# Kernel tuning notes

Hardware: AMD Instinct MI355X
Metric: run time of the kernel (lower is better)

## Reference

```python
import jax, jax.numpy as jnp
import numpy as np

B, S, D, H, L = 2, 2048, 512, 8, 4
DK = D // H
FFN = 2048
CHUNK, LEFT, RIGHT = 64, 128, 32
EPS = 1e-3  # keras LayerNormalization default epsilon
NEG_INF = -1.0e9


def _banded_mask():
    # chunk-local emformer mask: row i in chunk c attends to [c*CHUNK-LEFT, (c+1)*CHUNK+RIGHT)
    m = np.zeros((S, S), np.int32)
    for c in range(S // CHUNK):
        r0, r1 = c * CHUNK, (c + 1) * CHUNK
        c0, c1 = max(0, r0 - LEFT), min(S, r1 + RIGHT)
        m[r0:r1, c0:c1] = 1
    return jnp.asarray(np.broadcast_to(m[None, None], (B, 1, S, S)))


def setup_inputs() -> dict:
    key = jax.random.key(0)
    ks = jax.random.split(key, 8)
    sd = 1.0 / np.sqrt(D)
    inp = {
        "x": jax.random.normal(ks[0], (B, S, D), jnp.float32),
        "mask": _banded_mask(),
        "Wq": jax.random.normal(ks[1], (L, D, D), jnp.float32) * sd,
        "bq": jnp.zeros((L, D), jnp.float32),
        "Wk": jax.random.normal(ks[2], (L, D, D), jnp.float32) * sd,
        "bk": jnp.zeros((L, D), jnp.float32),
        "Wv": jax.random.normal(ks[3], (L, D, D), jnp.float32) * sd,
        "bv": jnp.zeros((L, D), jnp.float32),
        "W1": jax.random.normal(ks[4], (L, D, FFN), jnp.float32) * sd,
        "b1": jnp.zeros((L, FFN), jnp.float32),
        "W2": jax.random.normal(ks[5], (L, FFN, D), jnp.float32) / np.sqrt(FFN),
        "b2": jnp.zeros((L, D), jnp.float32),
        "ln_in_g": jnp.ones((L, D), jnp.float32),
        "ln_in_b": jnp.zeros((L, D), jnp.float32),
        "ln1_g": jnp.ones((L, D), jnp.float32),
        "ln1_b": jnp.zeros((L, D), jnp.float32),
        "ln2_g": jnp.ones((L, D), jnp.float32),
        "ln2_b": jnp.zeros((L, D), jnp.float32),
    }
    return inp


def _ln(x, g, b):
    mu = jnp.mean(x, axis=-1, keepdims=True)
    var = jnp.mean(jnp.square(x - mu), axis=-1, keepdims=True)
    return (x - mu) * jax.lax.rsqrt(var + EPS) * g + b


def _block(x, maskf, Wq, bq, Wk, bk, Wv, bv, W1, b1, W2, b2, g_in, b_in, g1, bb1, g2, bb2):
    bs = x.shape[0]
    xl = _ln(x, g_in, b_in)
    q = (xl @ Wq + bq).reshape(bs, -1, H, DK).transpose(0, 2, 1, 3)  # [B,H,S,dk]
    k = (xl @ Wk + bk).reshape(bs, -1, H, DK).transpose(0, 2, 1, 3)
    v = (xl @ Wv + bv).reshape(bs, -1, H, DK).transpose(0, 2, 1, 3)
    scores = jnp.einsum("bhsd,bhtd->bhst", q, k) / np.sqrt(DK)
    scores = scores + NEG_INF * (1.0 - maskf)
    probs = jax.nn.softmax(scores, axis=-1)
    out = jnp.einsum("bhst,bhtd->bhsd", probs, v)
    out = out.transpose(0, 2, 1, 3).reshape(bs, -1, H * DK)
    out = out + x  # residual to block input (pre-LN)
    attn_out = _ln(out, g1, bb1)
    ffn = jax.nn.relu(attn_out @ W1 + b1) @ W2 + b2
    return _ln(ffn + attn_out, g2, bb2)


def reference(x, mask, Wq, bq, Wk, bk, Wv, bv, W1, b1, W2, b2,
              ln_in_g, ln_in_b, ln1_g, ln1_b, ln2_g, ln2_b):
    maskf = mask.astype(x.dtype)
    for i in range(L):
        x = _block(x, maskf, Wq[i], bq[i], Wk[i], bk[i], Wv[i], bv[i],
                   W1[i], b1[i], W2[i], b2[i],
                   ln_in_g[i], ln_in_b[i], ln1_g[i], ln1_b[i], ln2_g[i], ln2_b[i])
    return x
```

## Files before the change

### kernel.cpp

```cpp
#include <hip/hip_runtime.h>
#include <stdint.h>

#define DEVI __device__ __forceinline__

typedef __attribute__((ext_vector_type(8))) short bf16x8;
typedef __attribute__((ext_vector_type(4))) float f32x4;

DEVI short tobf(float v){
  uint32_t u = __builtin_bit_cast(uint32_t, v);
  uint32_t r = (u + 0x7fffu + ((u >> 16) & 1u)) >> 16;
  return (short)(uint16_t)r;
}

DEVI float frombf(short s){
  uint32_t u = ((uint32_t)(uint16_t)s) << 16;
  return __builtin_bit_cast(float, u);
}

DEVI f32x4 mfma16(bf16x8 a, bf16x8 b, f32x4 c){
  return __builtin_amdgcn_mfma_f32_16x16x32_bf16(a, b, c, 0, 0, 0);
}

DEVI void async16(const void* g, void* lds_uniform){
  __builtin_amdgcn_global_load_lds(
      (const __attribute__((address_space(1))) unsigned int*)g,
      (__attribute__((address_space(3))) unsigned int*)lds_uniform,
      16, 0, 0);
}

DEVI void ln_row_compute(const float* __restrict__ in, const short* __restrict__ inb,
                         const float* __restrict__ resf, const short* __restrict__ resb,
                         const float* __restrict__ g, const float* __restrict__ be,
                         const float* __restrict__ gn, const float* __restrict__ bn,
                         float* __restrict__ outf, short* __restrict__ outb, int row)
{
  const int lane = threadIdx.x & 63;
  const size_t base = (size_t)row * 512 + lane * 8;
  const int col = lane * 8;
  f32x4 x0, x1;
  if (in){
    x0 = *(const f32x4*)(in + base);
    x1 = *(const f32x4*)(in + base + 4);
  } else {
    bf16x8 ib = *(const bf16x8*)(inb + base);
    #pragma unroll
    for (int i = 0; i < 4; i++){ x0[i] = frombf(ib[i]); x1[i] = frombf(ib[i+4]); }
  }
  if (resf){
    f32x4 r0v = *(const f32x4*)(resf + base), r1v = *(const f32x4*)(resf + base + 4);
    x0 += r0v; x1 += r1v;
  }
  if (resb){
    bf16x8 rb = *(const bf16x8*)(resb + base);
    #pragma unroll
    for (int i = 0; i < 4; i++){ x0[i] += frombf(rb[i]); x1[i] += frombf(rb[i+4]); }
  }
  float s = x0[0]+x0[1]+x0[2]+x0[3]+x1[0]+x1[1]+x1[2]+x1[3];
  #pragma unroll
  for (int m = 1; m < 64; m <<= 1) s += __shfl_xor(s, m, 64);
  const float mu = s * (1.f/512.f);
  float vs = 0.f;
  #pragma unroll
  for (int i = 0; i < 4; i++){
    float d0 = x0[i]-mu; vs += d0*d0;
    float d1 = x1[i]-mu; vs += d1*d1;
  }
  #pragma unroll
  for (int m = 1; m < 64; m <<= 1) vs += __shfl_xor(vs, m, 64);
  const float rs = rsqrtf(vs * (1.f/512.f) + 1e-3f);
  f32x4 gv0 = *(const f32x4*)(g+col),  gv1 = *(const f32x4*)(g+col+4);
  f32x4 bv0 = *(const f32x4*)(be+col), bv1 = *(const f32x4*)(be+col+4);
  f32x4 y0, y1;
  #pragma unroll
  for (int i = 0; i < 4; i++){
    y0[i] = (x0[i]-mu)*rs*gv0[i] + bv0[i];
    y1[i] = (x1[i]-mu)*rs*gv1[i] + bv1[i];
  }
  if (outf){ *(f32x4*)(outf+base) = y0; *(f32x4*)(outf+base+4) = y1; }
  if (outb){
    f32x4 z0 = y0, z1 = y1;
    if (gn){
      float s2 = z0[0]+z0[1]+z0[2]+z0[3]+z1[0]+z1[1]+z1[2]+z1[3];
      #pragma unroll
      for (int m = 1; m < 64; m <<= 1) s2 += __shfl_xor(s2, m, 64);
      const float mu2 = s2 * (1.f/512.f);
      float v2 = 0.f;
      #pragma unroll
      for (int i = 0; i < 4; i++){
        float d0 = z0[i]-mu2; v2 += d0*d0;
        float d1 = z1[i]-mu2; v2 += d1*d1;
      }
      #pragma unroll
      for (int m = 1; m < 64; m <<= 1) v2 += __shfl_xor(v2, m, 64);
      const float rs2 = rsqrtf(v2 * (1.f/512.f) + 1e-3f);
      f32x4 gn0 = *(const f32x4*)(gn+col), gn1 = *(const f32x4*)(gn+col+4);
      f32x4 bn0 = *(const f32x4*)(bn+col), bn1 = *(const f32x4*)(bn+col+4);
      #pragma unroll
      for (int i = 0; i < 4; i++){
        z0[i] = (z0[i]-mu2)*rs2*gn0[i] + bn0[i];
        z1[i] = (z1[i]-mu2)*rs2*gn1[i] + bn1[i];
      }
    }
    bf16x8 ob;
    #pragma unroll
    for (int i = 0; i < 4; i++){ ob[i] = tobf(z0[i]); ob[i+4] = tobf(z1[i]); }
    *(bf16x8*)(outb + base) = ob;
  }
}

__global__ __launch_bounds__(256)
void transpose_all(const float* __restrict__ Wq, const float* __restrict__ Wk,
                   const float* __restrict__ Wv, const float* __restrict__ W1,
                   const float* __restrict__ W2,
                   short* __restrict__ WqkvT, short* __restrict__ W1T,
                   short* __restrict__ W2T,
                   const float* __restrict__ x_in, const float* __restrict__ gin,
                   const float* __restrict__ bin, short* __restrict__ xl)
{
  if (blockIdx.x >= 11264){
    const int row = ((blockIdx.x - 11264) << 2) + (threadIdx.x >> 6);
    ln_row_compute(x_in, nullptr, nullptr, nullptr, gin, bin,
                   nullptr, nullptr, nullptr, xl, row);
    return;
  }
  __shared__ float tsh[32][33];
  const int l = blockIdx.x / 2816;
  const int t = blockIdx.x % 2816;
  const float* src; short* dst; int K, N, local;
  if (t < 768){
    const int m = t >> 8;
    src = (m==0 ? Wq : (m==1 ? Wk : Wv)) + (size_t)l*262144;
    dst = WqkvT + (size_t)l*786432 + m*262144; K = 512; N = 512; local = t & 255;
  } else if (t < 1792){
    src = W1 + (size_t)l*1048576; dst = W1T + (size_t)l*1048576;
    K = 512; N = 2048; local = t - 768;
  } else {
    src = W2 + (size_t)l*1048576; dst = W2T + (size_t)l*1048576;
    K = 2048; N = 512; local = t - 1792;
  }
  const int tnx = N >> 5;
  const int tc = (local % tnx) << 5, tr = (local / tnx) << 5;
  const int lr = threadIdx.x >> 5, lc = threadIdx.x & 31;
  #pragma unroll
  for (int i = 0; i < 32; i += 8)
    tsh[lr + i][lc] = src[(size_t)(tr + lr + i) * N + tc + lc];
  __syncthreads();
  #pragma unroll
  for (int i = 0; i < 32; i += 8)
    dst[(size_t)(tc + lr + i) * K + tr + lc] = tobf(tsh[lc][lr + i]);
}

__global__ __launch_bounds__(256)
void ln_kernel(const float* __restrict__ in, const short* __restrict__ inb,
               const float* __restrict__ resf, const short* __restrict__ resb,
               const float* __restrict__ g, const float* __restrict__ be,
               const float* __restrict__ gn, const float* __restrict__ bn,
               float* __restrict__ outf, short* __restrict__ outb)
{
  const int row = (blockIdx.x << 2) + (threadIdx.x >> 6);
  ln_row_compute(in, inb, resf, resb, g, be, gn, bn, outf, outb, row);
}

template<int MODE, int BJ, int BK>
__global__ __launch_bounds__(256)
void gemm_bt(const short* __restrict__ A, const short* __restrict__ BT,
             int N, int K,
             const float* __restrict__ b0, const float* __restrict__ b1p,
             const float* __restrict__ b2p, void* __restrict__ out0)
{
  constexpr int NTILE = 32*BJ;
  constexpr int UPR = BK/8;
  constexpr int AU = 64*UPR/256;
  constexpr int BU = NTILE*UPR/256;
  __shared__ __align__(16) short Ash[64*BK];
  __shared__ __align__(16) short Bsh[NTILE*BK];
  const int tid = threadIdx.x;
  const int wid = tid >> 6, lane = tid & 63;
  const int l15 = lane & 15, g4 = lane >> 4;
  const int nbn = N / NTILE;
  const int cpx = gridDim.x >> 3;
  int bid = blockIdx.x;
  bid = (bid & 7) * cpx + (bid >> 3);
  const int bm = bid / nbn, bn = bid % nbn;
  const int m0 = bm << 6, n0 = bn * NTILE;

  const short* aP[AU]; const short* bP[BU];
  #pragma unroll
  for (int p = 0; p < AU; p++){
    int u = p*256 + tid, row = u / UPR, sl = (u % UPR) ^ (row & (UPR-1));
    aP[p] = A + (size_t)(m0 + row) * K + sl * 8;
  }
  #pragma unroll
  for (int p = 0; p < BU; p++){
    int u = p*256 + tid, row = u / UPR, sl = (u % UPR) ^ (row & (UPR-1));
    bP[p] = BT + (size_t)(n0 + row) * K + sl * 8;
  }
  char* ldsA = (char*)Ash;
  char* ldsB = (char*)Bsh;

  f32x4 acc[2][BJ] = {};
  const int wr = wid & 1, wc = wid >> 1;
  const int nkt = K / BK;

  for (int kt = 0; kt < nkt; ++kt){
    const int k0 = kt * BK;
    #pragma unroll
    for (int p = 0; p < AU; p++)
      async16(aP[p] + k0, ldsA + (p*256 + wid*64) * 16);
    #pragma unroll
    for (int p = 0; p < BU; p++)
      async16(bP[p] + k0, ldsB + (p*256 + wid*64) * 16);
    __syncthreads();
    #pragma unroll
    for (int ks = 0; ks < BK/32; ++ks){
      bf16x8 af[2], bfm[BJ];
      #pragma unroll
      for (int i = 0; i < 2; i++){
        const int ar = wr*32 + i*16 + l15;
        af[i] = *(const bf16x8*)&ldsA[ar*(2*BK) + (((ks<<2)+g4) ^ (ar&(UPR-1)))*16];
      }
      #pragma unroll
      for (int j = 0; j < BJ; j++){
        const int br = wc*(16*BJ) + j*16 + l15;
        bfm[j] = *(const bf16x8*)&ldsB[br*(2*BK) + (((ks<<2)+g4) ^ (br&(UPR-1)))*16];
      }
      #pragma unroll
      for (int i = 0; i < 2; i++)
        #pragma unroll
        for (int j = 0; j < BJ; j++)
          acc[i][j] = mfma16(af[i], bfm[j], acc[i][j]);
    }
    __syncthreads();
  }

  const int r0 = m0 + wr*32 + g4*4;
  const int cc0 = n0 + wc*16*BJ + l15;
  #pragma unroll
  for (int j = 0; j < BJ; j++){
    const int gc = cc0 + j*16;
    if (MODE == 0){
      const float bi = gc < 512 ? b0[gc] : (gc < 1024 ? b1p[gc-512] : b2p[gc-1024]);
      short* ob = (short*)out0;
      #pragma unroll
      for (int i = 0; i < 2; i++)
        #pragma unroll
        for (int r = 0; r < 4; r++){
          const int grow = r0 + i*16 + r;
          ob[(size_t)grow * N + gc] = tobf(acc[i][j][r] + bi);
        }
    } else {
      const float bi = b0[gc];
      short* ob = (short*)out0;
      #pragma unroll
      for (int i = 0; i < 2; i++)
        #pragma unroll
        for (int r = 0; r < 4; r++){
          const int grow = r0 + i*16 + r;
          float v = acc[i][j][r] + bi;
          v = fmaxf(v, 0.f);
          ob[(size_t)grow * N + gc] = tobf(v);
        }
    }
  }
}

__global__ __launch_bounds__(256)
void attn_kernel(const short* __restrict__ qkv, short* __restrict__ attnO,
                 const float* __restrict__ resid)
{
  constexpr int NT = 14, NK2 = 7, VS = 232, LDQ = 1536;
  __shared__ __align__(16) short Vt[64*VS];
  __shared__ __align__(16) short Pl[4][16*VS];
  const int c = blockIdx.x, h = blockIdx.y, b = blockIdx.z;
  const int kb0 = 64*c - 128;
  const size_t rowbase = (size_t)b*2048;
  const short* Q     = qkv + (rowbase + 64*c)*LDQ + h*64;
  const short* Kbase = qkv + rowbase*LDQ + 512  + h*64;
  const short* Vbase = qkv + rowbase*LDQ + 1024 + h*64;
  const int tid = threadIdx.x, wid = tid >> 6, lane = tid & 63;
  const int l15 = lane & 15, g4 = lane >> 4;

  for (int idx = tid; idx < NT*16*8; idx += 256){
    const int t = idx >> 7, rem = idx & 127;
    const int r = rem >> 3, d8 = (rem & 7) << 3;
    const int kb = kb0 + t*16;
    bf16x8 v = {0,0,0,0,0,0,0,0};
    if (kb >= 0 && kb + 16 <= 2048)
      v = *(const bf16x8*)(Vbase + (size_t)(kb + r)*LDQ + d8);
    short* dst = &Vt[d8*VS + t*16 + r];
    #pragma unroll
    for (int e = 0; e < 8; e++) dst[e*VS] = v[e];
  }

  const short* qr = Q + (wid*16 + l15)*LDQ + g4*8;
  const bf16x8 aq0 = *(const bf16x8*)qr;
  const bf16x8 aq1 = *(const bf16x8*)(qr + 32);

  f32x4 sf[NT];
  #pragma unroll
  for (int t = 0; t < NT; t++){
    const int kb = kb0 + t*16;
    if (kb >= 0 && kb + 16 <= 2048){
      const short* kr = Kbase + (size_t)(kb + l15)*LDQ + g4*8;
      const bf16x8 k0 = *(const bf16x8*)kr;
      const bf16x8 k1 = *(const bf16x8*)(kr + 32);
      f32x4 z = {0.f,0.f,0.f,0.f};
      z = mfma16(aq0, k0, z);
      z = mfma16(aq1, k1, z);
      sf[t] = z;
    } else {
      sf[t] = (f32x4){-1e9f,-1e9f,-1e9f,-1e9f};
    }
  }

  float mx[4] = {-1e30f,-1e30f,-1e30f,-1e30f};
  #pragma unroll
  for (int t = 0; t < NT; t++)
    #pragma unroll
    for (int r = 0; r < 4; r++) mx[r] = fmaxf(mx[r], sf[t][r]);
  #pragma unroll
  for (int m = 1; m < 16; m <<= 1)
    #pragma unroll
    for (int r = 0; r < 4; r++) mx[r] = fmaxf(mx[r], __shfl_xor(mx[r], m, 64));

  float sum[4] = {0.f,0.f,0.f,0.f};
  #pragma unroll
  for (int t = 0; t < NT; t++)
    #pragma unroll
    for (int r = 0; r < 4; r++){
      const float p = __expf((sf[t][r] - mx[r]) * 0.125f);
      sf[t][r] = p; sum[r] += p;
    }
  #pragma unroll
  for (int m = 1; m < 16; m <<= 1)
    #pragma unroll
    for (int r = 0; r < 4; r++) sum[r] += __shfl_xor(sum[r], m, 64);
  float inv[4];
  #pragma unroll
  for (int r = 0; r < 4; r++) inv[r] = 1.f / sum[r];

  short* Pw = Pl[wid];
  #pragma unroll
  for (int t = 0; t < NT; t++)
    #pragma unroll
    for (int r = 0; r < 4; r++)
      Pw[(g4*4 + r)*VS + t*16 + l15] = tobf(sf[t][r]);

  __syncthreads();

  f32x4 ao[4] = {};
  #pragma unroll
  for (int ks = 0; ks < NK2; ks++){
    const bf16x8 pa = *(const bf16x8*)&Pw[l15*VS + ks*32 + g4*8];
    #pragma unroll
    for (int ni = 0; ni < 4; ni++){
      const bf16x8 vb = *(const bf16x8*)&Vt[(ni*16 + l15)*VS + ks*32 + g4*8];
      ao[ni] = mfma16(pa, vb, ao[ni]);
    }
  }

  const int orow = 64*c + wid*16 + g4*4;
  const size_t obase = ((size_t)b*2048 + orow)*512 + h*64;
  short* ob = attnO + obase;
  const float* rb = resid + obase;
  #pragma unroll
  for (int ni = 0; ni < 4; ni++)
    #pragma unroll
    for (int r = 0; r < 4; r++)
      ob[(size_t)r*512 + ni*16 + l15] =
          tobf(ao[ni][r] * inv[r] + rb[(size_t)r*512 + ni*16 + l15]);
}

extern "C" void kernel_launch(void* const* d_in, const int* in_sizes, int n_in,
                              void* d_out, int out_size, void* d_ws, size_t ws_size,
                              hipStream_t stream)
{
  const float* x_in = (const float*)d_in[0];
  const float* Wq = (const float*)d_in[2];
  const float* bq = (const float*)d_in[3];
  const float* Wk = (const float*)d_in[4];
  const float* bk = (const float*)d_in[5];
  const float* Wv = (const float*)d_in[6];
  const float* bv = (const float*)d_in[7];
  const float* W1 = (const float*)d_in[8];
  const float* b1 = (const float*)d_in[9];
  const float* W2 = (const float*)d_in[10];
  const float* b2 = (const float*)d_in[11];
  const float* gin = (const float*)d_in[12];
  const float* bin = (const float*)d_in[13];
  const float* g1  = (const float*)d_in[14];
  const float* be1 = (const float*)d_in[15];
  const float* g2  = (const float*)d_in[16];
  const float* be2 = (const float*)d_in[17];

  char* ws = (char*)d_ws;
  size_t o = 0;
  float* xbuf  = (float*)(ws + o); o += (size_t)4096*512*4;
  short* xl    = (short*)(ws + o); o += (size_t)4096*512*2;
  short* qkv   = (short*)(ws + o); o += (size_t)4096*1536*2;
  short* attnO = (short*)(ws + o); o += (size_t)4096*512*2;
  short* h1    = (short*)(ws + o); o += (size_t)4096*2048*2;
  short* f2out = (short*)(ws + o); o += (size_t)4096*512*2;
  short* WqkvT = (short*)(ws + o); o += (size_t)4*1536*512*2;
  short* W1T   = (short*)(ws + o); o += (size_t)4*2048*512*2;
  short* W2T   = (short*)(ws + o); o += (size_t)4*512*2048*2;

  transpose_all<<<12288,256,0,stream>>>(Wq, Wk, Wv, W1, W2, WqkvT, W1T, W2T,
                                        x_in, gin, bin, xl);

  for (int l = 0; l < 4; l++){
    gemm_bt<0,3,128><<<1024,256,0,stream>>>(xl, WqkvT + (size_t)l*786432, 1536, 512,
                                            bq + l*512, bk + l*512, bv + l*512, qkv);
    attn_kernel<<<dim3(32,8,2),256,0,stream>>>(qkv, attnO, l == 0 ? x_in : xbuf);
    ln_kernel<<<1024,256,0,stream>>>(nullptr, attnO, nullptr, nullptr,
                                     g1 + l*512, be1 + l*512, nullptr, nullptr,
                                     nullptr, xl);
    gemm_bt<1,4,64><<<1024,256,0,stream>>>(xl, W1T + (size_t)l*1048576, 2048, 512,
                                           b1 + l*2048, nullptr, nullptr, h1);
    gemm_bt<0,2,256><<<512,256,0,stream>>>(h1, W2T + (size_t)l*1048576, 512, 2048,
                                           b2 + l*512, nullptr, nullptr, f2out);
    if (l < 3){
      ln_kernel<<<1024,256,0,stream>>>(nullptr, f2out, nullptr, xl,
                                       g2 + l*512, be2 + l*512,
                                       gin + (l+1)*512, bin + (l+1)*512,
                                       xbuf, xl);
    } else {
      ln_kernel<<<1024,256,0,stream>>>(nullptr, f2out, nullptr, xl,
                                       g2 + l*512, be2 + l*512,
                                       nullptr, nullptr, (float*)d_out, nullptr);
    }
  }
}
```

Baseline: 285.4 us.

## Split-K the FFN down-projection and fold partial sums into LayerNorm

```diff
diff --git a/kernel.cpp b/kernel.cpp
--- a/kernel.cpp
+++ b/kernel.cpp
@@ -30,6 +30,7 @@
 
 DEVI void ln_row_compute(const float* __restrict__ in, const short* __restrict__ inb,
                          const float* __restrict__ resf, const short* __restrict__ resb,
+                         const float* __restrict__ cb,
                          const float* __restrict__ g, const float* __restrict__ be,
                          const float* __restrict__ gn, const float* __restrict__ bn,
                          float* __restrict__ outf, short* __restrict__ outb, int row)
@@ -55,6 +56,10 @@
     #pragma unroll
     for (int i = 0; i < 4; i++){ x0[i] += frombf(rb[i]); x1[i] += frombf(rb[i+4]); }
   }
+  if (cb){
+    f32x4 c0 = *(const f32x4*)(cb + col), c1 = *(const f32x4*)(cb + col + 4);
+    x0 += c0; x1 += c1;
+  }
   float s = x0[0]+x0[1]+x0[2]+x0[3]+x1[0]+x1[1]+x1[2]+x1[3];
   #pragma unroll
   for (int m = 1; m < 64; m <<= 1) s += __shfl_xor(s, m, 64);
@@ -119,7 +124,7 @@
 {
   if (blockIdx.x >= 11264){
     const int row = ((blockIdx.x - 11264) << 2) + (threadIdx.x >> 6);
-    ln_row_compute(x_in, nullptr, nullptr, nullptr, gin, bin,
+    ln_row_compute(x_in, nullptr, nullptr, nullptr, nullptr, gin, bin,
                    nullptr, nullptr, nullptr, xl, row);
     return;
   }
@@ -153,18 +158,19 @@
 __global__ __launch_bounds__(256)
 void ln_kernel(const float* __restrict__ in, const short* __restrict__ inb,
                const float* __restrict__ resf, const short* __restrict__ resb,
+               const float* __restrict__ cb,
                const float* __restrict__ g, const float* __restrict__ be,
                const float* __restrict__ gn, const float* __restrict__ bn,
                float* __restrict__ outf, short* __restrict__ outb)
 {
   const int row = (blockIdx.x << 2) + (threadIdx.x >> 6);
-  ln_row_compute(in, inb, resf, resb, g, be, gn, bn, outf, outb, row);
+  ln_row_compute(in, inb, resf, resb, cb, g, be, gn, bn, outf, outb, row);
 }
 
 template<int MODE, int BJ, int BK>
 __global__ __launch_bounds__(256)
 void gemm_bt(const short* __restrict__ A, const short* __restrict__ BT,
-             int N, int K,
+             int N, int K, int Ks,
              const float* __restrict__ b0, const float* __restrict__ b1p,
              const float* __restrict__ b2p, void* __restrict__ out0)
 {
@@ -183,24 +189,25 @@
   bid = (bid & 7) * cpx + (bid >> 3);
   const int bm = bid / nbn, bn = bid % nbn;
   const int m0 = bm << 6, n0 = bn * NTILE;
+  const int kofs = blockIdx.z * Ks;
 
   const short* aP[AU]; const short* bP[BU];
   #pragma unroll
   for (int p = 0; p < AU; p++){
     int u = p*256 + tid, row = u / UPR, sl = (u % UPR) ^ (row & (UPR-1));
-    aP[p] = A + (size_t)(m0 + row) * K + sl * 8;
+    aP[p] = A + (size_t)(m0 + row) * K + kofs + sl * 8;
   }
   #pragma unroll
   for (int p = 0; p < BU; p++){
     int u = p*256 + tid, row = u / UPR, sl = (u % UPR) ^ (row & (UPR-1));
-    bP[p] = BT + (size_t)(n0 + row) * K + sl * 8;
+    bP[p] = BT + (size_t)(n0 + row) * K + kofs + sl * 8;
   }
   char* ldsA = (char*)Ash;
   char* ldsB = (char*)Bsh;
 
   f32x4 acc[2][BJ] = {};
   const int wr = wid & 1, wc = wid >> 1;
-  const int nkt = K / BK;
+  const int nkt = Ks / BK;
 
   for (int kt = 0; kt < nkt; ++kt){
     const int k0 = kt * BK;
@@ -248,7 +255,7 @@
           const int grow = r0 + i*16 + r;
           ob[(size_t)grow * N + gc] = tobf(acc[i][j][r] + bi);
         }
-    } else {
+    } else if (MODE == 1){
       const float bi = b0[gc];
       short* ob = (short*)out0;
       #pragma unroll
@@ -259,6 +266,15 @@
           float v = acc[i][j][r] + bi;
           v = fmaxf(v, 0.f);
           ob[(size_t)grow * N + gc] = tobf(v);
+        }
+    } else {
+      float* ob = (float*)out0 + (size_t)blockIdx.z * 2097152;
+      #pragma unroll
+      for (int i = 0; i < 2; i++)
+        #pragma unroll
+        for (int r = 0; r < 4; r++){
+          const int grow = r0 + i*16 + r;
+          ob[(size_t)grow * N + gc] = acc[i][j][r];
         }
     }
   }
@@ -400,7 +416,7 @@
   short* qkv   = (short*)(ws + o); o += (size_t)4096*1536*2;
   short* attnO = (short*)(ws + o); o += (size_t)4096*512*2;
   short* h1    = (short*)(ws + o); o += (size_t)4096*2048*2;
-  short* f2out = (short*)(ws + o); o += (size_t)4096*512*2;
+  float* pbuf  = (float*)(ws + o); o += (size_t)2*4096*512*4;
   short* WqkvT = (short*)(ws + o); o += (size_t)4*1536*512*2;
   short* W1T   = (short*)(ws + o); o += (size_t)4*2048*512*2;
   short* W2T   = (short*)(ws + o); o += (size_t)4*512*2048*2;
@@ -409,23 +425,23 @@
                                         x_in, gin, bin, xl);
 
   for (int l = 0; l < 4; l++){
-    gemm_bt<0,3,128><<<1024,256,0,stream>>>(xl, WqkvT + (size_t)l*786432, 1536, 512,
+    gemm_bt<0,3,128><<<1024,256,0,stream>>>(xl, WqkvT + (size_t)l*786432, 1536, 512, 512,
                                             bq + l*512, bk + l*512, bv + l*512, qkv);
     attn_kernel<<<dim3(32,8,2),256,0,stream>>>(qkv, attnO, l == 0 ? x_in : xbuf);
-    ln_kernel<<<1024,256,0,stream>>>(nullptr, attnO, nullptr, nullptr,
+    ln_kernel<<<1024,256,0,stream>>>(nullptr, attnO, nullptr, nullptr, nullptr,
                                      g1 + l*512, be1 + l*512, nullptr, nullptr,
                                      nullptr, xl);
-    gemm_bt<1,4,64><<<1024,256,0,stream>>>(xl, W1T + (size_t)l*1048576, 2048, 512,
+    gemm_bt<1,2,64><<<2048,256,0,stream>>>(xl, W1T + (size_t)l*1048576, 2048, 512, 512,
                                            b1 + l*2048, nullptr, nullptr, h1);
-    gemm_bt<0,2,256><<<512,256,0,stream>>>(h1, W2T + (size_t)l*1048576, 512, 2048,
-                                           b2 + l*512, nullptr, nullptr, f2out);
+    gemm_bt<3,2,128><<<dim3(512,1,2),256,0,stream>>>(h1, W2T + (size_t)l*1048576, 512, 2048, 1024,
+                                                     nullptr, nullptr, nullptr, pbuf);
     if (l < 3){
-      ln_kernel<<<1024,256,0,stream>>>(nullptr, f2out, nullptr, xl,
+      ln_kernel<<<1024,256,0,stream>>>(pbuf, nullptr, pbuf + 2097152, xl, b2 + l*512,
                                        g2 + l*512, be2 + l*512,
                                        gin + (l+1)*512, bin + (l+1)*512,
                                        xbuf, xl);
     } else {
-      ln_kernel<<<1024,256,0,stream>>>(nullptr, f2out, nullptr, xl,
+      ln_kernel<<<1024,256,0,stream>>>(pbuf, nullptr, pbuf + 2097152, xl, b2 + l*512,
                                        g2 + l*512, be2 + l*512,
                                        nullptr, nullptr, (float*)d_out, nullptr);
     }
```

Result: slower. 302.0 us (+5.8%).
